# Kernel optimization log

Measured on AMD Instinct MI355X. Metric: run time of the kernel, lower is better.

## Reference

```python
import jax, jax.numpy as jnp
import numpy as np
import math

DIM_V = 512
NUM_HEADS = 8
LN_EPS = 1e-5


def _layer_norm(x, g, b):
    mu = jnp.mean(x, axis=-1, keepdims=True)
    var = jnp.mean(jnp.square(x - mu), axis=-1, keepdims=True)
    return (x - mu) * jax.lax.rsqrt(var + LN_EPS) * g + b


def setup_inputs() -> dict:
    key = jax.random.key(0)
    ks = jax.random.split(key, 12)
    B, Nq, Nk, Dq, Dk, Dv = 16, 1024, 1024, 512, 512, DIM_V
    s_q = 1.0 / math.sqrt(Dq)
    s_k = 1.0 / math.sqrt(Dk)
    s_v = 1.0 / math.sqrt(Dv)
    return {
        "Q": jax.random.normal(ks[0], (B, Nq, Dq), jnp.float32),
        "K": jax.random.normal(ks[1], (B, Nk, Dk), jnp.float32),
        "Wq": jax.random.normal(ks[2], (Dq, Dv), jnp.float32) * s_q,
        "bq": jnp.zeros((Dv,), jnp.float32),
        "Wk": jax.random.normal(ks[3], (Dk, Dv), jnp.float32) * s_k,
        "bk": jnp.zeros((Dv,), jnp.float32),
        "Wv": jax.random.normal(ks[4], (Dk, Dv), jnp.float32) * s_k,
        "bv": jnp.zeros((Dv,), jnp.float32),
        "Wo": jax.random.normal(ks[5], (Dv, Dv), jnp.float32) * s_v,
        "bo": jnp.zeros((Dv,), jnp.float32),
        "g0": jnp.ones((Dv,), jnp.float32),
        "b0": jnp.zeros((Dv,), jnp.float32),
        "g1": jnp.ones((Dv,), jnp.float32),
        "b1": jnp.zeros((Dv,), jnp.float32),
    }


def reference(Q, K, Wq, bq, Wk, bk, Wv, bv, Wo, bo, g0, b0, g1, b1):
    B, Nq, _ = Q.shape
    H = NUM_HEADS
    hd = DIM_V // H
    Qp = Q @ Wq + bq            # [B, Nq, Dv]
    Kp = K @ Wk + bk            # [B, Nk, Dv]
    Vp = K @ Wv + bv            # [B, Nk, Dv]
    # split heads: [B, N, H, hd]
    Qh = Qp.reshape(B, Nq, H, hd)
    Kh = Kp.reshape(B, -1, H, hd)
    Vh = Vp.reshape(B, -1, H, hd)
    # NOTE: original scales by sqrt(dim_V), not sqrt(head_dim)
    scores = jnp.einsum("bqhd,bkhd->bhqk", Qh, Kh) / math.sqrt(DIM_V)
    A = jax.nn.softmax(scores, axis=-1)          # [B, H, Nq, Nk]
    Oh = Qh + jnp.einsum("bhqk,bkhd->bqhd", A, Vh)  # residual on projected Q
    O = Oh.reshape(B, Nq, DIM_V)
    O = _layer_norm(O, g0, b0)
    O = O + jax.nn.relu(O @ Wo + bo)
    O = _layer_norm(O, g1, b1)
    return O
```

## Files before the change

kernel.cpp:

```cpp
#include <hip/hip_runtime.h>
#include <hip/hip_bf16.h>

typedef float f32x4 __attribute__((ext_vector_type(4)));
typedef __bf16 bf16x8 __attribute__((ext_vector_type(8)));
typedef __bf16 bf16x4 __attribute__((ext_vector_type(4)));

#define MFMA(a, b, c) __builtin_amdgcn_mfma_f32_16x16x32_bf16(a, b, c, 0, 0, 0)
#define AS1 __attribute__((address_space(1)))
#define AS3 __attribute__((address_space(3)))

__device__ __forceinline__ void gload16(const unsigned short* g, unsigned short* l) {
    __builtin_amdgcn_global_load_lds((const AS1 unsigned int*)g, (AS3 unsigned int*)l, 16, 0, 0);
}

__device__ __forceinline__ unsigned short f2bf(float f) {
    union { float f; unsigned u; } x{f};
    unsigned r = x.u + 0x7FFFu + ((x.u >> 16) & 1u);
    return (unsigned short)(r >> 16);
}
__device__ __forceinline__ float bf2f(unsigned short u) {
    union { unsigned u; float f; } x; x.u = ((unsigned)u) << 16; return x.f;
}

__global__ __launch_bounds__(256) void k_cvt2(const float* __restrict__ Q,
                                              const float* __restrict__ K,
                                              unsigned short* __restrict__ out) {
    int bid = blockIdx.x;
    const float* in = (bid < 4096) ? Q : K;
    size_t off = (size_t)(bid >> 12) * 8388608;
    int i = ((bid & 4095) * 256 + threadIdx.x) * 8;
    float4 a = *(const float4*)(in + i);
    float4 b = *(const float4*)(in + i + 4);
    union { unsigned short u[8]; int4 v; } r;
    r.u[0] = f2bf(a.x); r.u[1] = f2bf(a.y); r.u[2] = f2bf(a.z); r.u[3] = f2bf(a.w);
    r.u[4] = f2bf(b.x); r.u[5] = f2bf(b.y); r.u[6] = f2bf(b.z); r.u[7] = f2bf(b.w);
    *(int4*)(out + off + i) = r.v;
}

__global__ __launch_bounds__(256) void k_transpose4(const float* W0, const float* W1,
                                                    const float* W2, const float* W3,
                                                    unsigned short* T0, unsigned short* T1,
                                                    unsigned short* T2, unsigned short* T3) {
    __shared__ float T[64][65];
    int sel = blockIdx.x >> 6, tile = blockIdx.x & 63;
    const float* W = sel == 0 ? W0 : sel == 1 ? W1 : sel == 2 ? W2 : W3;
    unsigned short* Wt = sel == 0 ? T0 : sel == 1 ? T1 : sel == 2 ? T2 : T3;
    int k0 = (tile >> 3) * 64, n0 = (tile & 7) * 64;
    int tid = threadIdx.x;
    for (int it = 0; it < 16; ++it) {
        int id = it * 256 + tid;
        int r = id >> 6, c = id & 63;
        T[r][c] = W[(k0 + r) * 512 + n0 + c];
    }
    __syncthreads();
    for (int it = 0; it < 16; ++it) {
        int id = it * 256 + tid;
        int r = id >> 6, c = id & 63;
        Wt[(n0 + r) * 512 + k0 + c] = f2bf(T[c][r]);
    }
}

template <int MODE>
__global__ __launch_bounds__(256) void k_gemm(const unsigned short* __restrict__ A,
                                              const unsigned short* __restrict__ Bt,
                                              const float* __restrict__ bias,
                                              void* __restrict__ outp,
                                              float scale) {
    __shared__ __align__(16) unsigned short smem[16384];
    const int tid = threadIdx.x;
    const int lane = tid & 63, w = tid >> 6;
    int ib = blockIdx.x;
    const int mt = (ib & 7) | ((ib >> 5) << 3), nt = (ib >> 3) & 3;
    const int m0 = mt * 128, n0 = nt * 128;
    const int wm = (w >> 1) * 64, wn = (w & 1) * 64;
    const int l15 = lane & 15, l4 = lane >> 4;

    const f32x4 vz = {0.f, 0.f, 0.f, 0.f};
    f32x4 acc[4][4];
    for (int i = 0; i < 4; ++i)
        for (int j = 0; j < 4; ++j) acc[i][j] = vz;

    const unsigned short* Abase = A + (size_t)m0 * 512;
    const unsigned short* Bbase = Bt + (size_t)n0 * 512;

    auto STAGE = [&](int ks, int p) {
        int kk = ks * 32;
        for (int it = 0; it < 2; ++it) {
            int id = it * 256 + tid;
            int r = id >> 2, x = id & 3, c = x ^ (r & 3);
            unsigned short* ldsb = smem + p * 4096 + (it * 256 + w * 64) * 8;
            gload16(Abase + r * 512 + kk + c * 8, ldsb);
            gload16(Bbase + r * 512 + kk + c * 8, ldsb + 8192);
        }
    };

    STAGE(0, 0);
    __syncthreads();
    for (int ks = 0; ks < 16; ++ks) {
        int p = ks & 1;
        if (ks < 15) STAGE(ks + 1, p ^ 1);
        const unsigned short* Ab = smem + p * 4096;
        const unsigned short* Bb = smem + 8192 + p * 4096;
        bf16x8 af[4], bfr[4];
        for (int i = 0; i < 4; ++i) {
            int r = wm + i * 16 + l15, pc = l4 ^ (r & 3);
            af[i] = *(const bf16x8*)&Ab[r * 32 + pc * 8];
        }
        for (int j = 0; j < 4; ++j) {
            int r = wn + j * 16 + l15, pc = l4 ^ (r & 3);
            bfr[j] = *(const bf16x8*)&Bb[r * 32 + pc * 8];
        }
        __builtin_amdgcn_s_setprio(1);
        for (int i = 0; i < 4; ++i)
            for (int j = 0; j < 4; ++j)
                acc[i][j] = MFMA(af[i], bfr[j], acc[i][j]);
        __builtin_amdgcn_s_setprio(0);
        __syncthreads();
    }

    float bn[4];
    for (int j = 0; j < 4; ++j) bn[j] = bias[n0 + wn + j * 16 + l15];

    if constexpr (MODE == 0) {
        unsigned short* out = (unsigned short*)outp;
        for (int i = 0; i < 4; ++i)
            for (int j = 0; j < 4; ++j)
                for (int rg = 0; rg < 4; ++rg) {
                    int m = m0 + wm + i * 16 + l4 * 4 + rg;
                    int n = n0 + wn + j * 16 + l15;
                    out[(size_t)m * 512 + n] = f2bf((acc[i][j][rg] + bn[j]) * scale);
                }
    } else {
        unsigned short* T = smem + w * 4096;
        for (int i = 0; i < 4; ++i)
            for (int j = 0; j < 4; ++j)
                for (int rg = 0; rg < 4; ++rg) {
                    int ml = i * 16 + l4 * 4 + rg;
                    int nl = j * 16 + l15;
                    int pc = (ml >> 3) ^ (nl & 7);
                    T[nl * 64 + pc * 8 + (ml & 7)] = f2bf(acc[i][j][rg] + bn[j]);
                }
        unsigned short* out = (unsigned short*)outp;
        int b = (m0 + wm) >> 10;
        int key0 = (m0 + wm) & 1023;
        for (int it = 0; it < 8; ++it) {
            int ch = it * 64 + lane;
            int nl = ch >> 3, c = ch & 7, pc = c ^ (nl & 7);
            int4 v = *(const int4*)&T[nl * 64 + pc * 8];
            int d = n0 + wn + nl;
            *(int4*)(out + ((size_t)b * 512 + d) * 1024 + key0 + c * 8) = v;
        }
    }
}

__global__ __launch_bounds__(256) void k_attn(const unsigned short* __restrict__ Qs,
                                              const unsigned short* __restrict__ Kp,
                                              const unsigned short* __restrict__ VpT,
                                              unsigned short* __restrict__ O1b) {
    __shared__ __align__(16) unsigned short sm[20480];
    const int tid = threadIdx.x, lane = tid & 63, w = tid >> 6;
    const int l15 = lane & 15, l4 = lane >> 4;
    int i = blockIdx.x;
    const int qt = (i >> 3) & 15;
    const int hb = (i & 7) | ((i >> 7) << 3);
    const int h = hb & 7, b = hb >> 3;
    const int q0 = qt * 64 + w * 16;

    const unsigned short* Ksrc = Kp + (size_t)(b * 1024) * 512 + h * 64;
    const unsigned short* Vsrc = VpT + (size_t)(b * 512 + h * 64) * 1024;
    const unsigned short* qrow = Qs + (size_t)(b * 1024 + q0 + l15) * 512 + h * 64;

    bf16x8 aq[2];
    aq[0] = *(const bf16x8*)(qrow + l4 * 8);
    aq[1] = *(const bf16x8*)(qrow + 32 + l4 * 8);

    const f32x4 vz = {0.f, 0.f, 0.f, 0.f};
    f32x4 acc[4];
    for (int t = 0; t < 4; ++t) acc[t] = vz;
    f32x4 ls = vz;

    char* Pb = (char*)(sm + 16384 + w * 1024) + l15 * 128;
    const int pswz = (l15 & 7) << 4;

    auto STAGE = [&](int kv, int p) {
        for (int it = 0; it < 2; ++it) {
            int id = it * 256 + tid;
            int r = id >> 3, x = id & 7, c = x ^ (r & 7);
            unsigned short* ldsb = sm + p * 4096 + (it * 256 + w * 64) * 8;
            gload16(Ksrc + (size_t)(kv * 64 + r) * 512 + c * 8, ldsb);
            gload16(Vsrc + (size_t)r * 1024 + kv * 64 + c * 8, ldsb + 8192);
        }
    };

    STAGE(0, 0);
    __syncthreads();
    for (int kv = 0; kv < 16; ++kv) {
        int p = kv & 1;
        if (kv < 15) STAGE(kv + 1, p ^ 1);
        const unsigned short* Kl = sm + p * 4096;
        const unsigned short* Vl = sm + 8192 + p * 4096;

        f32x4 s[4];
        for (int sub = 0; sub < 4; ++sub) s[sub] = vz;
        __builtin_amdgcn_s_setprio(1);
        for (int sub = 0; sub < 4; ++sub)
            for (int jj = 0; jj < 2; ++jj) {
                int r = sub * 16 + l15, c = jj * 4 + l4, pc = c ^ (r & 7);
                bf16x8 kf = *(const bf16x8*)&Kl[r * 64 + pc * 8];
                s[sub] = MFMA(kf, aq[jj], s[sub]);
            }
        __builtin_amdgcn_s_setprio(0);

        for (int sub = 0; sub < 4; ++sub) {
            for (int rg = 0; rg < 4; ++rg)
                s[sub][rg] = __builtin_amdgcn_exp2f(s[sub][rg]);
            ls += s[sub];
        }

        for (int sub = 0; sub < 4; ++sub) {
            bf16x4 pv = {(__bf16)s[sub][0], (__bf16)s[sub][1], (__bf16)s[sub][2], (__bf16)s[sub][3]};
            *(bf16x4*)(Pb + (((sub * 32 + l4 * 8)) ^ pswz)) = pv;
        }
        bf16x8 pf0 = *(const bf16x8*)(Pb + ((l4 * 16) ^ pswz));
        bf16x8 pf1 = *(const bf16x8*)(Pb + ((64 + l4 * 16) ^ pswz));
        __builtin_amdgcn_s_setprio(1);
        for (int sub2 = 0; sub2 < 4; ++sub2) {
            int r = sub2 * 16 + l15;
            int pc0 = l4 ^ (r & 7), pc1 = (4 + l4) ^ (r & 7);
            bf16x8 vf0 = *(const bf16x8*)&Vl[r * 64 + pc0 * 8];
            bf16x8 vf1 = *(const bf16x8*)&Vl[r * 64 + pc1 * 8];
            acc[sub2] = MFMA(vf0, pf0, acc[sub2]);
            acc[sub2] = MFMA(vf1, pf1, acc[sub2]);
        }
        __builtin_amdgcn_s_setprio(0);
        __syncthreads();
    }

    float lr = (ls[0] + ls[1]) + (ls[2] + ls[3]);
    lr += __shfl_xor(lr, 16);
    lr += __shfl_xor(lr, 32);
    const float invscale = 15.6841306f;
    float linv = 1.0f / lr;
    unsigned short* orow = O1b + (size_t)(b * 1024 + q0 + l15) * 512 + h * 64;
    for (int sub2 = 0; sub2 < 4; ++sub2) {
        bf16x4 qres = *(const bf16x4*)(qrow + sub2 * 16 + l4 * 4);
        bf16x4 ov;
        for (int rg = 0; rg < 4; ++rg)
            ov[rg] = (__bf16)((float)qres[rg] * invscale + acc[sub2][rg] * linv);
        *(bf16x4*)(orow + sub2 * 16 + l4 * 4) = ov;
    }
}

__global__ __launch_bounds__(256) void k_ln_bf(const unsigned short* __restrict__ in,
                                               unsigned short* __restrict__ outb,
                                               const float* __restrict__ g,
                                               const float* __restrict__ bt) {
    int row = blockIdx.x * 4 + (threadIdx.x >> 6);
    int lane = threadIdx.x & 63;
    const unsigned short* x = in + (size_t)row * 512 + lane * 8;
    bf16x8 v = *(const bf16x8*)x;
    float f[8];
    for (int j = 0; j < 8; ++j) f[j] = (float)v[j];
    float s1 = 0.f, s2 = 0.f;
    for (int j = 0; j < 8; ++j) { s1 += f[j]; s2 += f[j] * f[j]; }
    for (int off = 32; off; off >>= 1) {
        s1 += __shfl_xor(s1, off);
        s2 += __shfl_xor(s2, off);
    }
    float mu = s1 * (1.f / 512.f);
    float var = s2 * (1.f / 512.f) - mu * mu;
    float rs = rsqrtf(var + 1e-5f);
    float4 ga = *(const float4*)(g + lane * 8), gb = *(const float4*)(g + lane * 8 + 4);
    float4 ba = *(const float4*)(bt + lane * 8), bb = *(const float4*)(bt + lane * 8 + 4);
    float gg[8] = {ga.x, ga.y, ga.z, ga.w, gb.x, gb.y, gb.z, gb.w};
    float bv[8] = {ba.x, ba.y, ba.z, ba.w, bb.x, bb.y, bb.z, bb.w};
    bf16x8 y;
    for (int j = 0; j < 8; ++j) y[j] = (__bf16)((f[j] - mu) * rs * gg[j] + bv[j]);
    *(bf16x8*)(outb + (size_t)row * 512 + lane * 8) = y;
}

__global__ __launch_bounds__(512, 2) void k_gemm2ln(const unsigned short* __restrict__ A,
                                                    const unsigned short* __restrict__ Bt,
                                                    const float* __restrict__ bias,
                                                    const float* __restrict__ g1,
                                                    const float* __restrict__ b1,
                                                    float* __restrict__ out) {
    __shared__ __align__(16) unsigned short Ab[2][2048];
    __shared__ __align__(16) unsigned short Bb[2][16384];
    __shared__ float part[64][4][2];
    __shared__ float stats[64][2];
    const int tid = threadIdx.x, lane = tid & 63, w = tid >> 6;
    const int l15 = lane & 15, l4 = lane >> 4;
    const int m0 = blockIdx.x * 64;
    const int wm = (w >> 2) * 32, wn = (w & 3) * 128;

    const f32x4 vz = {0.f, 0.f, 0.f, 0.f};
    f32x4 acc[2][8];
    for (int i = 0; i < 2; ++i)
        for (int j = 0; j < 8; ++j) acc[i][j] = vz;

    const unsigned short* Abase = A + (size_t)m0 * 512;

    auto STAGE = [&](int ks, int p) {
        int kk = ks * 32;
        for (int it = 0; it < 4; ++it) {
            int id = it * 512 + tid;
            int r = id >> 2, x = id & 3, c = x ^ (r & 3);
            gload16(Bt + r * 512 + kk + c * 8, &Bb[p][(it * 512 + w * 64) * 8]);
        }
        if (w < 4) {
            int id = w * 64 + lane;
            int r = id >> 2, x = id & 3, c = x ^ (r & 3);
            gload16(Abase + r * 512 + kk + c * 8, &Ab[p][(w * 64) * 8]);
        }
    };

    STAGE(0, 0);
    __syncthreads();
    for (int ks = 0; ks < 16; ++ks) {
        int p = ks & 1;
        if (ks < 15) STAGE(ks + 1, p ^ 1);
        bf16x8 af[2], bfr[8];
        for (int i = 0; i < 2; ++i) {
            int r = wm + i * 16 + l15, pc = l4 ^ (r & 3);
            af[i] = *(const bf16x8*)&Ab[p][r * 32 + pc * 8];
        }
        for (int j = 0; j < 8; ++j) {
            int r = wn + j * 16 + l15, pc = l4 ^ (r & 3);
            bfr[j] = *(const bf16x8*)&Bb[p][r * 32 + pc * 8];
        }
        __builtin_amdgcn_s_setprio(1);
        for (int i = 0; i < 2; ++i)
            for (int j = 0; j < 8; ++j)
                acc[i][j] = MFMA(af[i], bfr[j], acc[i][j]);
        __builtin_amdgcn_s_setprio(0);
        __syncthreads();
    }

    float bn[8], gv[8], bv2[8];
    for (int j = 0; j < 8; ++j) {
        int n = wn + j * 16 + l15;
        bn[j] = bias[n]; gv[j] = g1[n]; bv2[j] = b1[n];
    }
    f32x4 s1v[2], s2v[2];
    for (int i = 0; i < 2; ++i) { s1v[i] = vz; s2v[i] = vz; }
    for (int i = 0; i < 2; ++i)
        for (int j = 0; j < 8; ++j)
            for (int rg = 0; rg < 4; ++rg) {
                int row = m0 + wm + i * 16 + l4 * 4 + rg;
                int n = wn + j * 16 + l15;
                float z = acc[i][j][rg] + bn[j];
                z = z > 0.f ? z : 0.f;
                float v = bf2f(A[(size_t)row * 512 + n]) + z;
                acc[i][j][rg] = v;
                s1v[i][rg] += v;
                s2v[i][rg] += v * v;
            }
    for (int i = 0; i < 2; ++i)
        for (int rg = 0; rg < 4; ++rg) {
            float a = s1v[i][rg], c = s2v[i][rg];
            for (int off = 1; off < 16; off <<= 1) {
                a += __shfl_xor(a, off);
                c += __shfl_xor(c, off);
            }
            s1v[i][rg] = a; s2v[i][rg] = c;
        }
    if (l15 == 0)
        for (int i = 0; i < 2; ++i)
            for (int rg = 0; rg < 4; ++rg) {
                int rl = wm + i * 16 + l4 * 4 + rg;
                part[rl][w & 3][0] = s1v[i][rg];
                part[rl][w & 3][1] = s2v[i][rg];
            }
    __syncthreads();
    if (tid < 64) {
        float a = 0.f, c = 0.f;
        for (int q = 0; q < 4; ++q) { a += part[tid][q][0]; c += part[tid][q][1]; }
        float mu = a * (1.f / 512.f);
        float var = c * (1.f / 512.f) - mu * mu;
        stats[tid][0] = mu;
        stats[tid][1] = rsqrtf(var + 1e-5f);
    }
    __syncthreads();
    for (int i = 0; i < 2; ++i)
        for (int rg = 0; rg < 4; ++rg) {
            int rl = wm + i * 16 + l4 * 4 + rg;
            float mu = stats[rl][0], rs = stats[rl][1];
            for (int j = 0; j < 8; ++j) {
                int n = wn + j * 16 + l15;
                out[(size_t)(m0 + rl) * 512 + n] = (acc[i][j][rg] - mu) * rs * gv[j] + bv2[j];
            }
        }
}

extern "C" void kernel_launch(void* const* d_in, const int* in_sizes, int n_in,
                              void* d_out, int out_size, void* d_ws, size_t ws_size,
                              hipStream_t stream) {
    const float* Q  = (const float*)d_in[0];
    const float* K  = (const float*)d_in[1];
    const float* Wq = (const float*)d_in[2];
    const float* bq = (const float*)d_in[3];
    const float* Wk = (const float*)d_in[4];
    const float* bk = (const float*)d_in[5];
    const float* Wv = (const float*)d_in[6];
    const float* bv = (const float*)d_in[7];
    const float* Wo = (const float*)d_in[8];
    const float* bo = (const float*)d_in[9];
    const float* g0 = (const float*)d_in[10];
    const float* b0 = (const float*)d_in[11];
    const float* g1 = (const float*)d_in[12];
    const float* b1 = (const float*)d_in[13];
    float* out = (float*)d_out;

    const size_t SZ_BF = (size_t)16384 * 512 * 2;
    const size_t SZ_W  = (size_t)512 * 512 * 2;
    char* p = (char*)d_ws;
    unsigned short* Qbf = (unsigned short*)p; p += SZ_BF;
    unsigned short* Kbf = (unsigned short*)p; p += SZ_BF;
    unsigned short* Wqt = (unsigned short*)p; p += SZ_W;
    unsigned short* Wkt = (unsigned short*)p; p += SZ_W;
    unsigned short* Wvt = (unsigned short*)p; p += SZ_W;
    unsigned short* Wot = (unsigned short*)p; p += SZ_W;
    unsigned short* Qsc = (unsigned short*)p; p += SZ_BF;
    unsigned short* Kp  = (unsigned short*)p; p += SZ_BF;
    unsigned short* VpT = (unsigned short*)p; p += SZ_BF;
    unsigned short* A1b = (unsigned short*)p; p += SZ_BF;
    unsigned short* X0b = (unsigned short*)p; p += SZ_BF;

    k_cvt2<<<8192, 256, 0, stream>>>(Q, K, Qbf);
    k_transpose4<<<256, 256, 0, stream>>>(Wq, Wk, Wv, Wo, Wqt, Wkt, Wvt, Wot);

    const float scale2 = 0.063758718f;
    k_gemm<0><<<512, 256, 0, stream>>>(Qbf, Wqt, bq, Qsc, scale2);
    k_gemm<0><<<512, 256, 0, stream>>>(Kbf, Wkt, bk, Kp, 1.0f);
    k_gemm<1><<<512, 256, 0, stream>>>(Kbf, Wvt, bv, VpT, 1.0f);

    k_attn<<<2048, 256, 0, stream>>>(Qsc, Kp, VpT, A1b);

    k_ln_bf<<<4096, 256, 0, stream>>>(A1b, X0b, g0, b0);
    k_gemm2ln<<<256, 512, 0, stream>>>(X0b, Wot, bo, g1, b1, out);
}
```

Measured before the change: 150.3 us.

## Fuse fp32-to-bf16 conversion into projection GEMMs and use 32x32 MFMA attention

Removes the separate fp32→bf16 conversion kernel. The projection GEMMs now stage fp32 Q/K tiles straight into LDS and convert them while building the MFMA fragments. The attention kernel is rewritten to use 32x32x16 MFMA with 128-query tiles per block, halving the grid, and it stages P through a padded LDS buffer. The GEMM change trades one full read and write of the activations for twice the LDS traffic on the A operand. The attention change alters register pressure and occupancy.

```diff
diff --git a/kernel.cpp b/kernel.cpp
--- a/kernel.cpp
+++ b/kernel.cpp
@@ -2,14 +2,16 @@
 #include <hip/hip_bf16.h>
 
 typedef float f32x4 __attribute__((ext_vector_type(4)));
+typedef float f32x16 __attribute__((ext_vector_type(16)));
 typedef __bf16 bf16x8 __attribute__((ext_vector_type(8)));
 typedef __bf16 bf16x4 __attribute__((ext_vector_type(4)));
 
 #define MFMA(a, b, c) __builtin_amdgcn_mfma_f32_16x16x32_bf16(a, b, c, 0, 0, 0)
+#define MFMA32(a, b, c) __builtin_amdgcn_mfma_f32_32x32x16_bf16(a, b, c, 0, 0, 0)
 #define AS1 __attribute__((address_space(1)))
 #define AS3 __attribute__((address_space(3)))
 
-__device__ __forceinline__ void gload16(const unsigned short* g, unsigned short* l) {
+__device__ __forceinline__ void gload16(const void* g, void* l) {
     __builtin_amdgcn_global_load_lds((const AS1 unsigned int*)g, (AS3 unsigned int*)l, 16, 0, 0);
 }
 
@@ -20,21 +22,6 @@
 }
 __device__ __forceinline__ float bf2f(unsigned short u) {
     union { unsigned u; float f; } x; x.u = ((unsigned)u) << 16; return x.f;
-}
-
-__global__ __launch_bounds__(256) void k_cvt2(const float* __restrict__ Q,
-                                              const float* __restrict__ K,
-                                              unsigned short* __restrict__ out) {
-    int bid = blockIdx.x;
-    const float* in = (bid < 4096) ? Q : K;
-    size_t off = (size_t)(bid >> 12) * 8388608;
-    int i = ((bid & 4095) * 256 + threadIdx.x) * 8;
-    float4 a = *(const float4*)(in + i);
-    float4 b = *(const float4*)(in + i + 4);
-    union { unsigned short u[8]; int4 v; } r;
-    r.u[0] = f2bf(a.x); r.u[1] = f2bf(a.y); r.u[2] = f2bf(a.z); r.u[3] = f2bf(a.w);
-    r.u[4] = f2bf(b.x); r.u[5] = f2bf(b.y); r.u[6] = f2bf(b.z); r.u[7] = f2bf(b.w);
-    *(int4*)(out + off + i) = r.v;
 }
 
 __global__ __launch_bounds__(256) void k_transpose4(const float* W0, const float* W1,
@@ -61,12 +48,13 @@
 }
 
 template <int MODE>
-__global__ __launch_bounds__(256) void k_gemm(const unsigned short* __restrict__ A,
-                                              const unsigned short* __restrict__ Bt,
-                                              const float* __restrict__ bias,
-                                              void* __restrict__ outp,
-                                              float scale) {
-    __shared__ __align__(16) unsigned short smem[16384];
+__global__ __launch_bounds__(256) void k_gemmF(const float* __restrict__ A,
+                                               const unsigned short* __restrict__ Bt,
+                                               const float* __restrict__ bias,
+                                               void* __restrict__ outp,
+                                               float scale) {
+    __shared__ __align__(16) float AbS[2][4096];
+    __shared__ __align__(16) unsigned short BbS[2][4096];
     const int tid = threadIdx.x;
     const int lane = tid & 63, w = tid >> 6;
     int ib = blockIdx.x;
@@ -80,17 +68,22 @@
     for (int i = 0; i < 4; ++i)
         for (int j = 0; j < 4; ++j) acc[i][j] = vz;
 
-    const unsigned short* Abase = A + (size_t)m0 * 512;
+    const float* Abase = A + (size_t)m0 * 512;
     const unsigned short* Bbase = Bt + (size_t)n0 * 512;
 
     auto STAGE = [&](int ks, int p) {
         int kk = ks * 32;
+        #pragma unroll
+        for (int it = 0; it < 4; ++it) {
+            int id = it * 256 + tid;
+            int r = id >> 3, cc = id & 7, g = cc ^ (r & 7);
+            gload16(Abase + r * 512 + kk + g * 4, &AbS[p][(it * 256 + w * 64) * 4]);
+        }
+        #pragma unroll
         for (int it = 0; it < 2; ++it) {
             int id = it * 256 + tid;
             int r = id >> 2, x = id & 3, c = x ^ (r & 3);
-            unsigned short* ldsb = smem + p * 4096 + (it * 256 + w * 64) * 8;
-            gload16(Abase + r * 512 + kk + c * 8, ldsb);
-            gload16(Bbase + r * 512 + kk + c * 8, ldsb + 8192);
+            gload16(Bbase + r * 512 + kk + c * 8, &BbS[p][(it * 256 + w * 64) * 8]);
         }
     };
 
@@ -99,19 +92,26 @@
     for (int ks = 0; ks < 16; ++ks) {
         int p = ks & 1;
         if (ks < 15) STAGE(ks + 1, p ^ 1);
-        const unsigned short* Ab = smem + p * 4096;
-        const unsigned short* Bb = smem + 8192 + p * 4096;
         bf16x8 af[4], bfr[4];
+        #pragma unroll
         for (int i = 0; i < 4; ++i) {
-            int r = wm + i * 16 + l15, pc = l4 ^ (r & 3);
-            af[i] = *(const bf16x8*)&Ab[r * 32 + pc * 8];
-        }
+            int r = wm + i * 16 + l15;
+            int pc0 = (2 * l4) ^ (r & 7);
+            const float* Af = &AbS[p][r * 32];
+            f32x4 a0 = *(const f32x4*)(Af + pc0 * 4);
+            f32x4 a1 = *(const f32x4*)(Af + (pc0 ^ 1) * 4);
+            af[i] = bf16x8{(__bf16)a0[0], (__bf16)a0[1], (__bf16)a0[2], (__bf16)a0[3],
+                           (__bf16)a1[0], (__bf16)a1[1], (__bf16)a1[2], (__bf16)a1[3]};
+        }
+        #pragma unroll
         for (int j = 0; j < 4; ++j) {
             int r = wn + j * 16 + l15, pc = l4 ^ (r & 3);
-            bfr[j] = *(const bf16x8*)&Bb[r * 32 + pc * 8];
+            bfr[j] = *(const bf16x8*)&BbS[p][r * 32 + pc * 8];
         }
         __builtin_amdgcn_s_setprio(1);
+        #pragma unroll
         for (int i = 0; i < 4; ++i)
+            #pragma unroll
             for (int j = 0; j < 4; ++j)
                 acc[i][j] = MFMA(af[i], bfr[j], acc[i][j]);
         __builtin_amdgcn_s_setprio(0);
@@ -131,7 +131,8 @@
                     out[(size_t)m * 512 + n] = f2bf((acc[i][j][rg] + bn[j]) * scale);
                 }
     } else {
-        unsigned short* T = smem + w * 4096;
+        unsigned short* T = (unsigned short*)&AbS[0][0] + w * 4096;
+        __syncthreads();
         for (int i = 0; i < 4; ++i)
             for (int j = 0; j < 4; ++j)
                 for (int rg = 0; rg < 4; ++rg) {
@@ -153,36 +154,38 @@
     }
 }
 
-__global__ __launch_bounds__(256) void k_attn(const unsigned short* __restrict__ Qs,
-                                              const unsigned short* __restrict__ Kp,
-                                              const unsigned short* __restrict__ VpT,
-                                              unsigned short* __restrict__ O1b) {
-    __shared__ __align__(16) unsigned short sm[20480];
+__global__ __launch_bounds__(256) void k_attn32(const unsigned short* __restrict__ Qs,
+                                                const unsigned short* __restrict__ Kp,
+                                                const unsigned short* __restrict__ VpT,
+                                                unsigned short* __restrict__ O1b) {
+    __shared__ __align__(16) unsigned short sm[25600];
     const int tid = threadIdx.x, lane = tid & 63, w = tid >> 6;
-    const int l15 = lane & 15, l4 = lane >> 4;
+    const int l31 = lane & 31, hi = lane >> 5;
     int i = blockIdx.x;
-    const int qt = (i >> 3) & 15;
-    const int hb = (i & 7) | ((i >> 7) << 3);
-    const int h = hb & 7, b = hb >> 3;
-    const int q0 = qt * 64 + w * 16;
+    const int xcd = i & 7, jj = i >> 3;
+    const int qt = jj & 7, bhl = jj >> 3;
+    const int bh = xcd * 16 + bhl;
+    const int h = bh & 7, b = bh >> 3;
+    const int qrow = b * 1024 + qt * 128 + w * 32 + l31;
 
     const unsigned short* Ksrc = Kp + (size_t)(b * 1024) * 512 + h * 64;
     const unsigned short* Vsrc = VpT + (size_t)(b * 512 + h * 64) * 1024;
-    const unsigned short* qrow = Qs + (size_t)(b * 1024 + q0 + l15) * 512 + h * 64;
-
-    bf16x8 aq[2];
-    aq[0] = *(const bf16x8*)(qrow + l4 * 8);
-    aq[1] = *(const bf16x8*)(qrow + 32 + l4 * 8);
-
-    const f32x4 vz = {0.f, 0.f, 0.f, 0.f};
-    f32x4 acc[4];
-    for (int t = 0; t < 4; ++t) acc[t] = vz;
-    f32x4 ls = vz;
-
-    char* Pb = (char*)(sm + 16384 + w * 1024) + l15 * 128;
-    const int pswz = (l15 & 7) << 4;
+    const unsigned short* qptr = Qs + (size_t)qrow * 512 + h * 64;
+
+    bf16x8 qf[4];
+    #pragma unroll
+    for (int ks = 0; ks < 4; ++ks)
+        qf[ks] = *(const bf16x8*)(qptr + ks * 16 + hi * 8);
+
+    f32x16 acc0, acc1;
+    #pragma unroll
+    for (int r = 0; r < 16; ++r) { acc0[r] = 0.f; acc1[r] = 0.f; }
+    float ls = 0.f;
+
+    unsigned short* Pw = sm + 16384 + w * 2304;
 
     auto STAGE = [&](int kv, int p) {
+        #pragma unroll
         for (int it = 0; it < 2; ++it) {
             int id = it * 256 + tid;
             int r = id >> 3, x = id & 7, c = x ^ (r & 7);
@@ -199,55 +202,82 @@
         if (kv < 15) STAGE(kv + 1, p ^ 1);
         const unsigned short* Kl = sm + p * 4096;
         const unsigned short* Vl = sm + 8192 + p * 4096;
-
-        f32x4 s[4];
-        for (int sub = 0; sub < 4; ++sub) s[sub] = vz;
+        const int rsw = (l31 & 7);
+
+        f32x16 s0, s1;
+        #pragma unroll
+        for (int r = 0; r < 16; ++r) { s0[r] = 0.f; s1[r] = 0.f; }
         __builtin_amdgcn_s_setprio(1);
-        for (int sub = 0; sub < 4; ++sub)
-            for (int jj = 0; jj < 2; ++jj) {
-                int r = sub * 16 + l15, c = jj * 4 + l4, pc = c ^ (r & 7);
-                bf16x8 kf = *(const bf16x8*)&Kl[r * 64 + pc * 8];
-                s[sub] = MFMA(kf, aq[jj], s[sub]);
-            }
+        #pragma unroll
+        for (int ks = 0; ks < 4; ++ks) {
+            int c = (2 * ks + hi) ^ rsw;
+            bf16x8 kf0 = *(const bf16x8*)&Kl[l31 * 64 + c * 8];
+            s0 = MFMA32(kf0, qf[ks], s0);
+            bf16x8 kf1 = *(const bf16x8*)&Kl[(32 + l31) * 64 + c * 8];
+            s1 = MFMA32(kf1, qf[ks], s1);
+        }
         __builtin_amdgcn_s_setprio(0);
 
-        for (int sub = 0; sub < 4; ++sub) {
-            for (int rg = 0; rg < 4; ++rg)
-                s[sub][rg] = __builtin_amdgcn_exp2f(s[sub][rg]);
-            ls += s[sub];
-        }
-
-        for (int sub = 0; sub < 4; ++sub) {
-            bf16x4 pv = {(__bf16)s[sub][0], (__bf16)s[sub][1], (__bf16)s[sub][2], (__bf16)s[sub][3]};
-            *(bf16x4*)(Pb + (((sub * 32 + l4 * 8)) ^ pswz)) = pv;
-        }
-        bf16x8 pf0 = *(const bf16x8*)(Pb + ((l4 * 16) ^ pswz));
-        bf16x8 pf1 = *(const bf16x8*)(Pb + ((64 + l4 * 16) ^ pswz));
+        #pragma unroll
+        for (int g = 0; g < 4; ++g) {
+            float e0 = __builtin_amdgcn_exp2f(s0[4 * g + 0]);
+            float e1 = __builtin_amdgcn_exp2f(s0[4 * g + 1]);
+            float e2 = __builtin_amdgcn_exp2f(s0[4 * g + 2]);
+            float e3 = __builtin_amdgcn_exp2f(s0[4 * g + 3]);
+            float f0 = __builtin_amdgcn_exp2f(s1[4 * g + 0]);
+            float f1 = __builtin_amdgcn_exp2f(s1[4 * g + 1]);
+            float f2 = __builtin_amdgcn_exp2f(s1[4 * g + 2]);
+            float f3 = __builtin_amdgcn_exp2f(s1[4 * g + 3]);
+            ls += ((e0 + e1) + (e2 + e3)) + ((f0 + f1) + (f2 + f3));
+            bf16x4 pv0 = {(__bf16)e0, (__bf16)e1, (__bf16)e2, (__bf16)e3};
+            bf16x4 pv1 = {(__bf16)f0, (__bf16)f1, (__bf16)f2, (__bf16)f3};
+            *(bf16x4*)&Pw[l31 * 72 + 8 * g + 4 * hi] = pv0;
+            *(bf16x4*)&Pw[l31 * 72 + 32 + 8 * g + 4 * hi] = pv1;
+        }
+
+        bf16x8 pf[4];
+        #pragma unroll
+        for (int ks = 0; ks < 4; ++ks)
+            pf[ks] = *(const bf16x8*)&Pw[l31 * 72 + ks * 16 + hi * 8];
         __builtin_amdgcn_s_setprio(1);
-        for (int sub2 = 0; sub2 < 4; ++sub2) {
-            int r = sub2 * 16 + l15;
-            int pc0 = l4 ^ (r & 7), pc1 = (4 + l4) ^ (r & 7);
-            bf16x8 vf0 = *(const bf16x8*)&Vl[r * 64 + pc0 * 8];
-            bf16x8 vf1 = *(const bf16x8*)&Vl[r * 64 + pc1 * 8];
-            acc[sub2] = MFMA(vf0, pf0, acc[sub2]);
-            acc[sub2] = MFMA(vf1, pf1, acc[sub2]);
+        #pragma unroll
+        for (int ks = 0; ks < 4; ++ks) {
+            int c = (2 * ks + hi) ^ rsw;
+            bf16x8 vf0 = *(const bf16x8*)&Vl[l31 * 64 + c * 8];
+            acc0 = MFMA32(vf0, pf[ks], acc0);
+            bf16x8 vf1 = *(const bf16x8*)&Vl[(32 + l31) * 64 + c * 8];
+            acc1 = MFMA32(vf1, pf[ks], acc1);
         }
         __builtin_amdgcn_s_setprio(0);
         __syncthreads();
     }
 
-    float lr = (ls[0] + ls[1]) + (ls[2] + ls[3]);
-    lr += __shfl_xor(lr, 16);
-    lr += __shfl_xor(lr, 32);
+    ls += __shfl_xor(ls, 32);
+    float linv = 1.0f / ls;
     const float invscale = 15.6841306f;
-    float linv = 1.0f / lr;
-    unsigned short* orow = O1b + (size_t)(b * 1024 + q0 + l15) * 512 + h * 64;
-    for (int sub2 = 0; sub2 < 4; ++sub2) {
-        bf16x4 qres = *(const bf16x4*)(qrow + sub2 * 16 + l4 * 4);
-        bf16x4 ov;
-        for (int rg = 0; rg < 4; ++rg)
-            ov[rg] = (__bf16)((float)qres[rg] * invscale + acc[sub2][rg] * linv);
-        *(bf16x4*)(orow + sub2 * 16 + l4 * 4) = ov;
+    unsigned short* orow = O1b + (size_t)qrow * 512 + h * 64;
+    #pragma unroll
+    for (int g = 0; g < 4; ++g) {
+        {
+            int d0 = 8 * g + 4 * hi;
+            bf16x4 qres = *(const bf16x4*)(qptr + d0);
+            bf16x4 ov;
+            ov[0] = (__bf16)((float)qres[0] * invscale + acc0[4 * g + 0] * linv);
+            ov[1] = (__bf16)((float)qres[1] * invscale + acc0[4 * g + 1] * linv);
+            ov[2] = (__bf16)((float)qres[2] * invscale + acc0[4 * g + 2] * linv);
+            ov[3] = (__bf16)((float)qres[3] * invscale + acc0[4 * g + 3] * linv);
+            *(bf16x4*)(orow + d0) = ov;
+        }
+        {
+            int d0 = 32 + 8 * g + 4 * hi;
+            bf16x4 qres = *(const bf16x4*)(qptr + d0);
+            bf16x4 ov;
+            ov[0] = (__bf16)((float)qres[0] * invscale + acc1[4 * g + 0] * linv);
+            ov[1] = (__bf16)((float)qres[1] * invscale + acc1[4 * g + 1] * linv);
+            ov[2] = (__bf16)((float)qres[2] * invscale + acc1[4 * g + 2] * linv);
+            ov[3] = (__bf16)((float)qres[3] * invscale + acc1[4 * g + 3] * linv);
+            *(bf16x4*)(orow + d0) = ov;
+        }
     }
 }
 
@@ -415,8 +445,6 @@
     const size_t SZ_BF = (size_t)16384 * 512 * 2;
     const size_t SZ_W  = (size_t)512 * 512 * 2;
     char* p = (char*)d_ws;
-    unsigned short* Qbf = (unsigned short*)p; p += SZ_BF;
-    unsigned short* Kbf = (unsigned short*)p; p += SZ_BF;
     unsigned short* Wqt = (unsigned short*)p; p += SZ_W;
     unsigned short* Wkt = (unsigned short*)p; p += SZ_W;
     unsigned short* Wvt = (unsigned short*)p; p += SZ_W;
@@ -427,15 +455,14 @@
     unsigned short* A1b = (unsigned short*)p; p += SZ_BF;
     unsigned short* X0b = (unsigned short*)p; p += SZ_BF;
 
-    k_cvt2<<<8192, 256, 0, stream>>>(Q, K, Qbf);
     k_transpose4<<<256, 256, 0, stream>>>(Wq, Wk, Wv, Wo, Wqt, Wkt, Wvt, Wot);
 
     const float scale2 = 0.063758718f;
-    k_gemm<0><<<512, 256, 0, stream>>>(Qbf, Wqt, bq, Qsc, scale2);
-    k_gemm<0><<<512, 256, 0, stream>>>(Kbf, Wkt, bk, Kp, 1.0f);
-    k_gemm<1><<<512, 256, 0, stream>>>(Kbf, Wvt, bv, VpT, 1.0f);
-
-    k_attn<<<2048, 256, 0, stream>>>(Qsc, Kp, VpT, A1b);
+    k_gemmF<0><<<512, 256, 0, stream>>>(Q, Wqt, bq, Qsc, scale2);
+    k_gemmF<0><<<512, 256, 0, stream>>>(K, Wkt, bk, Kp, 1.0f);
+    k_gemmF<1><<<512, 256, 0, stream>>>(K, Wvt, bv, VpT, 1.0f);
+
+    k_attn32<<<1024, 256, 0, stream>>>(Qsc, Kp, VpT, A1b);
 
     k_ln_bf<<<4096, 256, 0, stream>>>(A1b, X0b, g0, b0);
     k_gemm2ln<<<256, 512, 0, stream>>>(X0b, Wot, bo, g1, b1, out);
```

After: 154.8 us. 3.0% more time.
